# Optimization experiments

Hardware: AMD Instinct MI355X
Metric: run time of the kernel (lower is better)

The kernel has to match this reference:

```python
import jax, jax.numpy as jnp
import numpy as np

NUM_BANDS = 30
SPLIT_FREQ = 30
M_PARAM = 1
DIM = 2048
BATCH = 16384


def _dct_mat(N):
    # Orthonormal DCT-II matrix D: dct(x) = x @ D.T, idct(y) = y @ D
    n = np.arange(N, dtype=np.float64)
    kk = n[:, None]
    M = np.cos(np.pi * (n + 0.5) * kk / N)
    s = np.full(N, np.sqrt(2.0 / N))
    s[0] = np.sqrt(1.0 / N)
    return jnp.asarray((M * s[:, None]).astype(np.float32))


def _band_scale(freq_weights, k, N):
    # Precompute the per-frequency scale vector the torch loop applies band-by-band.
    pts = np.linspace(0, N - 1, NUM_BANDS + 1).astype(np.int64)  # torch .long() truncation
    scale = jnp.ones((N,), dtype=freq_weights.dtype)
    for i in range(NUM_BANDS):
        s, e = int(pts[i]), int(pts[i + 1])
        if e <= SPLIT_FREQ:
            f = 1.0 + freq_weights[i] * k * (1.0 - i / NUM_BANDS)
        else:
            f = 1.0 - freq_weights[i] * k * (1.0 - (i - NUM_BANDS // M_PARAM) / NUM_BANDS)
        scale = scale.at[s:e].set(f)  # bands are disjoint; base is 1
    return scale


def setup_inputs() -> dict:
    key = jax.random.key(0)
    ks = jax.random.split(key, 6)
    g = 0.02  # small init like xavier_uniform with gain 0.5
    return {
        "x": jax.random.normal(ks[0], (BATCH, DIM), dtype=jnp.float32),
        "freq_weights": jnp.ones((NUM_BANDS,), dtype=jnp.float32),
        "k": jnp.float32(0.3),
        "W1": jax.random.normal(ks[1], (1024, DIM), dtype=jnp.float32) * g,
        "b1": jnp.zeros((1024,), dtype=jnp.float32),
        "W2": jax.random.normal(ks[2], (512, 1024), dtype=jnp.float32) * g,
        "b2": jnp.zeros((512,), dtype=jnp.float32),
        "Wmu": jax.random.normal(ks[3], (256, 512), dtype=jnp.float32) * g,
        "bmu": jnp.zeros((256,), dtype=jnp.float32),
        "Wlv": jax.random.normal(ks[4], (256, 512), dtype=jnp.float32) * g,
        "blv": jnp.zeros((256,), dtype=jnp.float32),
    }


def reference(x, freq_weights, k, W1, b1, W2, b2, Wmu, bmu, Wlv, blv):
    N = x.shape[-1]
    D = _dct_mat(N)
    # DCT -> per-band reweight -> IDCT, fused as two matmuls and one vector multiply
    xd = (x @ D.T) * _band_scale(freq_weights, k, N)
    xe = xd @ D
    h = jax.nn.relu(xe @ W1.T + b1)
    h = jax.nn.relu(h @ W2.T + b2)
    mu = h @ Wmu.T + bmu
    logvar = h @ Wlv.T + blv
    return (mu, logvar)
```

## Files before the change

kernel.cpp:

```cpp
#include <hip/hip_runtime.h>
#include <hip/hip_bf16.h>
#include <math.h>

#define DIM 2048
#define BATCH 16384

typedef __attribute__((ext_vector_type(8))) short short8;
typedef __attribute__((ext_vector_type(4))) short short4v;
typedef __attribute__((ext_vector_type(4))) float floatx4;
typedef unsigned short ushort_t;

__device__ __forceinline__ ushort_t f2bf(float f) {
    union { float f; unsigned u; } v; v.f = f;
    unsigned r = v.u + 0x7FFFu + ((v.u >> 16) & 1u);
    return (ushort_t)(r >> 16);
}

__global__ void k_scale(const float* __restrict__ fw, const float* __restrict__ kp,
                        float* __restrict__ s) {
    int n = blockIdx.x * blockDim.x + threadIdx.x;
    if (n >= DIM) return;
    float kv = kp[0];
    float f = 1.0f;
    for (int i = 0; i < 30; ++i) {
        long s0 = (long)((double)i       * (double)(DIM - 1) / 30.0);
        long e0 = (long)((double)(i + 1) * (double)(DIM - 1) / 30.0);
        if (n >= s0 && n < e0) {
            if (e0 <= 30)
                f = 1.0f + fw[i] * kv * (1.0f - (float)i / 30.0f);
            else
                f = 1.0f - fw[i] * kv * (1.0f - (float)(i - 30) / 30.0f);
        }
    }
    s[n] = f;
}

__global__ void k_gen_d(ushort_t* __restrict__ D, ushort_t* __restrict__ Dt) {
    int idx = blockIdx.x * blockDim.x + threadIdx.x;
    int r = idx >> 11;
    int c = idx & (DIM - 1);
    const float w  = 7.6699039394282058e-4f;
    const float s0 = 0.02209708691207961f;
    const float s1 = 0.03125f;
    int m1 = ((2 * c + 1) * r) & (4 * DIM - 1);
    int m2 = ((2 * r + 1) * c) & (4 * DIM - 1);
    float v1 = __cosf(w * (float)m1) * (r == 0 ? s0 : s1);
    float v2 = __cosf(w * (float)m2) * (c == 0 ? s0 : s1);
    D[idx]  = f2bf(v1);
    Dt[idx] = f2bf(v2);
}

#define U_W1   262144
#define U_W2    65536
#define U_WH    16384
__global__ void k_cast_w(const float* __restrict__ W1, const float* __restrict__ W2,
                         const float* __restrict__ Wmu, const float* __restrict__ Wlv,
                         ushort_t* __restrict__ W1bf, ushort_t* __restrict__ W2bf,
                         ushort_t* __restrict__ Wcat) {
    int i = blockIdx.x * blockDim.x + threadIdx.x;
    const float* src; ushort_t* dst; int u;
    if (i < U_W1)                    { src = W1;  dst = W1bf;             u = i; }
    else if (i < U_W1 + U_W2)        { src = W2;  dst = W2bf;             u = i - U_W1; }
    else if (i < U_W1 + U_W2 + U_WH) { src = Wmu; dst = Wcat;             u = i - U_W1 - U_W2; }
    else                             { src = Wlv; dst = Wcat + 8 * U_WH;  u = i - U_W1 - U_W2 - U_WH; }
    const float4* p = reinterpret_cast<const float4*>(src) + 2 * (size_t)u;
    float4 a = p[0], b = p[1];
    short8 r;
    r[0] = (short)f2bf(a.x); r[1] = (short)f2bf(a.y);
    r[2] = (short)f2bf(a.z); r[3] = (short)f2bf(a.w);
    r[4] = (short)f2bf(b.x); r[5] = (short)f2bf(b.y);
    r[6] = (short)f2bf(b.z); r[7] = (short)f2bf(b.w);
    *reinterpret_cast<short8*>(dst + 8 * (size_t)u) = r;
}

__global__ void k_cast_x(const float* __restrict__ in, ushort_t* __restrict__ out) {
    int i = blockIdx.x * blockDim.x + threadIdx.x;
    const float4* p = reinterpret_cast<const float4*>(in) + 2 * (size_t)i;
    float4 a = p[0], b = p[1];
    short8 r;
    r[0] = (short)f2bf(a.x); r[1] = (short)f2bf(a.y);
    r[2] = (short)f2bf(a.z); r[3] = (short)f2bf(a.w);
    r[4] = (short)f2bf(b.x); r[5] = (short)f2bf(b.y);
    r[6] = (short)f2bf(b.z); r[7] = (short)f2bf(b.w);
    *reinterpret_cast<short8*>(out + 8 * (size_t)i) = r;
}

__global__ void k_red(const float* __restrict__ P, ushort_t* __restrict__ out,
                      const float* __restrict__ scale, int n4, int n4row) {
    int i = blockIdx.x * blockDim.x + threadIdx.x;
    const float4* p = reinterpret_cast<const float4*>(P);
    float4 a = p[i], b = p[i + n4], c = p[i + 2 * n4], d = p[i + 3 * n4];
    float4 s;
    s.x = a.x + b.x + c.x + d.x;
    s.y = a.y + b.y + c.y + d.y;
    s.z = a.z + b.z + c.z + d.z;
    s.w = a.w + b.w + c.w + d.w;
    if (scale) {
        float4 sc = reinterpret_cast<const float4*>(scale)[i & (n4row - 1)];
        s.x *= sc.x; s.y *= sc.y; s.z *= sc.z; s.w *= sc.w;
    }
    short4v o;
    o[0] = (short)f2bf(s.x); o[1] = (short)f2bf(s.y);
    o[2] = (short)f2bf(s.z); o[3] = (short)f2bf(s.w);
    *reinterpret_cast<short4v*>(out + 4 * (size_t)i) = o;
}

template<int TM, int TN, int BK, int EPI, bool SK4>
__device__ __forceinline__ void gemm_core(
        const ushort_t* __restrict__ A, const ushort_t* __restrict__ B,
        ushort_t* __restrict__ Cb, float* __restrict__ Cf,
        const float* __restrict__ ep0, const float* __restrict__ ep1,
        int M, int N, int K, int KC) {
    constexpr int BM = 32 * TM;
    constexpr int BN = 32 * TN;
    constexpr int SEGS = BK / 8;
    constexpr int RSH  = (BK == 32) ? 1 : 0;
    constexpr int SSH  = (SEGS == 4) ? 2 : 3;
    __shared__ __align__(16) ushort_t As[BM * BK];
    __shared__ __align__(16) ushort_t Bs[BN * BK];

    const int tid  = threadIdx.x;
    const int lane = tid & 63;
    const int wave = tid >> 6;
    const int wm   = wave >> 1;
    const int wn   = wave & 1;
    const int q    = lane >> 4;
    const int l16  = lane & 15;

    const int tilesM = M / BM;
    const int tilesN = N / BN;
    int bid = (int)blockIdx.x;
    int sk = 0;
    if constexpr (SK4) { int nt = tilesM * tilesN; sk = bid / nt; bid = bid % nt; }
    const int xcd = bid & 7;
    const int j   = bid >> 3;
    const int bm  = xcd * (tilesM >> 3) + j / tilesN;
    const int bn  = j % tilesN;

    floatx4 acc[TM][TN];
    #pragma unroll
    for (int i = 0; i < TM; ++i)
        #pragma unroll
        for (int jj = 0; jj < TN; ++jj)
            acc[i][jj] = (floatx4){0.f, 0.f, 0.f, 0.f};

    const long aBase = (long)bm * BM * K + (long)sk * KC;
    const long bBase = (long)bn * BN * K + (long)sk * KC;
    const int  KLOOP = SK4 ? KC : K;

    for (int kt = 0; kt < KLOOP; kt += BK) {
        __syncthreads();
        #pragma unroll
        for (int i = 0; i < BM * BK / 2048; ++i) {
            int idx = tid + i * 256;
            int row = idx >> SSH, seg = idx & (SEGS - 1);
            int gseg = seg ^ ((row >> RSH) & (SEGS - 1));
            const ushort_t* g = A + aBase + (long)row * K + kt + gseg * 8;
            __builtin_amdgcn_global_load_lds(
                (const __attribute__((address_space(1))) void*)g,
                (__attribute__((address_space(3))) void*)(As + idx * 8),
                16, 0, 0);
        }
        #pragma unroll
        for (int i = 0; i < BN * BK / 2048; ++i) {
            int idx = tid + i * 256;
            int row = idx >> SSH, seg = idx & (SEGS - 1);
            int gseg = seg ^ ((row >> RSH) & (SEGS - 1));
            const ushort_t* g = B + bBase + (long)row * K + kt + gseg * 8;
            __builtin_amdgcn_global_load_lds(
                (const __attribute__((address_space(1))) void*)g,
                (__attribute__((address_space(3))) void*)(Bs + idx * 8),
                16, 0, 0);
        }
        __syncthreads();

        #pragma unroll
        for (int ks = 0; ks < BK / 32; ++ks) {
            short8 af[TM], bfr[TN];
            #pragma unroll
            for (int t = 0; t < TM; ++t) {
                int srow = wm * TM * 16 + t * 16 + l16;
                int rseg = (ks * 4 + q) ^ ((srow >> RSH) & (SEGS - 1));
                af[t] = *reinterpret_cast<const short8*>(&As[srow * BK + rseg * 8]);
            }
            #pragma unroll
            for (int t = 0; t < TN; ++t) {
                int srow = wn * TN * 16 + t * 16 + l16;
                int rseg = (ks * 4 + q) ^ ((srow >> RSH) & (SEGS - 1));
                bfr[t] = *reinterpret_cast<const short8*>(&Bs[srow * BK + rseg * 8]);
            }
            #pragma unroll
            for (int i = 0; i < TM; ++i)
                #pragma unroll
                for (int jj = 0; jj < TN; ++jj)
                    acc[i][jj] = __builtin_amdgcn_mfma_f32_16x16x32_bf16(
                        af[i], bfr[jj], acc[i][jj], 0, 0, 0);
        }
    }

    #pragma unroll
    for (int i = 0; i < TM; ++i) {
        #pragma unroll
        for (int jj = 0; jj < TN; ++jj) {
            #pragma unroll
            for (int r = 0; r < 4; ++r) {
                int row = bm * BM + wm * TM * 16 + i * 16 + q * 4 + r;
                int col = bn * BN + wn * TN * 16 + jj * 16 + l16;
                float v = acc[i][jj][r];
                if constexpr (EPI == 2) {
                    v += ep0[col];
                    v = v > 0.f ? v : 0.f;
                    Cb[(long)row * N + col] = f2bf(v);
                } else if constexpr (EPI == 3) {
                    const int half = N >> 1;
                    if (col < half)
                        Cf[(long)row * half + col] = v + ep0[col];
                    else
                        Cf[(long)M * half + (long)row * half + (col - half)] = v + ep1[col - half];
                } else {
                    Cf[(long)sk * M * N + (long)row * N + col] = v;
                }
            }
        }
    }
}


__global__ __launch_bounds__(512, 2) void g2_256(const ushort_t* __restrict__ A,
        const ushort_t* __restrict__ B, ushort_t* __restrict__ Cb,
        const float* __restrict__ bias, int M, int N, int K) {
    constexpr int BM = 256, BN = 256, BK = 32;
    __shared__ __align__(16) ushort_t As[4][BM * BK];
    __shared__ __align__(16) ushort_t Bs[4][BN * BK];

    const int tid  = threadIdx.x;
    const int lane = tid & 63;
    const int wave = tid >> 6;
    const int wm   = wave >> 2;
    const int wn   = wave & 3;
    const int q    = lane >> 4;
    const int l16  = lane & 15;

    const int tilesM = M / BM;
    const int tilesN = N / BN;
    int bid = (int)blockIdx.x;
    const int xcd = bid & 7;
    const int jb  = bid >> 3;
    const int bm  = xcd * (tilesM >> 3) + jb / tilesN;
    const int bn  = jb % tilesN;
    const int NT  = K / BK;

    const long aBase = (long)bm * BM * K;
    const long bBase = (long)bn * BN * K;

    floatx4 acc[8][4];
    #pragma unroll
    for (int i = 0; i < 8; ++i)
        #pragma unroll
        for (int j = 0; j < 4; ++j)
            acc[i][j] = (floatx4){0.f, 0.f, 0.f, 0.f};

#define STAGE_A(t) do { int _sl = (t) & 3;                                          \
        _Pragma("unroll")                                                           \
        for (int _g = 0; _g < 2; ++_g) {                                            \
            int _idx = _g * 512 + tid;                                              \
            int _row = _idx >> 2, _seg = _idx & 3;                                  \
            int _gs = _seg ^ ((_row >> 1) & 3);                                     \
            const ushort_t* _gp = A + aBase + (long)_row * K + (t) * BK + _gs * 8;  \
            __builtin_amdgcn_global_load_lds(                                       \
                (const __attribute__((address_space(1))) void*)_gp,                 \
                (__attribute__((address_space(3))) void*)(&As[_sl][_idx * 8]),      \
                16, 0, 0);                                                          \
        } } while (0)
#define STAGE_B(t) do { int _sl = (t) & 3;                                          \
        _Pragma("unroll")                                                           \
        for (int _g = 0; _g < 2; ++_g) {                                            \
            int _idx = _g * 512 + tid;                                              \
            int _row = _idx >> 2, _seg = _idx & 3;                                  \
            int _gs = _seg ^ ((_row >> 1) & 3);                                     \
            const ushort_t* _gp = B + bBase + (long)_row * K + (t) * BK + _gs * 8;  \
            __builtin_amdgcn_global_load_lds(                                       \
                (const __attribute__((address_space(1))) void*)_gp,                 \
                (__attribute__((address_space(3))) void*)(&Bs[_sl][_idx * 8]),      \
                16, 0, 0);                                                          \
        } } while (0)

    STAGE_A(0); STAGE_B(0);
    STAGE_A(1); STAGE_B(1);
    STAGE_A(2); STAGE_B(2);
    asm volatile("s_waitcnt vmcnt(8)" ::: "memory");
    __builtin_amdgcn_s_barrier();
    asm volatile("" ::: "memory");

#define KTILE(tt, DOSTAGE, WAITOP) do {                                             \
        const int _slot = (tt) & 3;                                                 \
        short8 _bf[4], _alo[4], _ahi[4];                                            \
        _Pragma("unroll")                                                           \
        for (int _j = 0; _j < 4; ++_j) {                                            \
            int _sr = wn * 64 + _j * 16 + l16;                                      \
            int _rs = q ^ ((_sr >> 1) & 3);                                         \
            _bf[_j] = *reinterpret_cast<const short8*>(&Bs[_slot][_sr * BK + _rs * 8]); \
        }                                                                           \
        _Pragma("unroll")                                                           \
        for (int _i = 0; _i < 4; ++_i) {                                            \
            int _sr = wm * 128 + _i * 16 + l16;                                     \
            int _rs = q ^ ((_sr >> 1) & 3);                                         \
            _alo[_i] = *reinterpret_cast<const short8*>(&As[_slot][_sr * BK + _rs * 8]); \
        }                                                                           \
        _Pragma("unroll")                                                           \
        for (int _i = 0; _i < 4; ++_i) {                                            \
            int _sr = wm * 128 + 64 + _i * 16 + l16;                                \
            int _rs = q ^ ((_sr >> 1) & 3);                                         \
            _ahi[_i] = *reinterpret_cast<const short8*>(&As[_slot][_sr * BK + _rs * 8]); \
        }                                                                           \
        if (DOSTAGE) { STAGE_A((tt) + 3); STAGE_B((tt) + 3); }                      \
        __builtin_amdgcn_s_setprio(1);                                              \
        _Pragma("unroll")                                                           \
        for (int _i = 0; _i < 4; ++_i)                                              \
            _Pragma("unroll")                                                       \
            for (int _j = 0; _j < 4; ++_j)                                          \
                acc[_i][_j] = __builtin_amdgcn_mfma_f32_16x16x32_bf16(              \
                    _alo[_i], _bf[_j], acc[_i][_j], 0, 0, 0);                       \
        _Pragma("unroll")                                                           \
        for (int _i = 0; _i < 4; ++_i)                                              \
            _Pragma("unroll")                                                       \
            for (int _j = 0; _j < 4; ++_j)                                          \
                acc[4 + _i][_j] = __builtin_amdgcn_mfma_f32_16x16x32_bf16(          \
                    _ahi[_i], _bf[_j], acc[4 + _i][_j], 0, 0, 0);                   \
        __builtin_amdgcn_s_setprio(0);                                              \
        asm volatile("s_waitcnt lgkmcnt(0)" ::: "memory");                          \
        __builtin_amdgcn_sched_barrier(0);                                          \
        WAITOP;                                                                     \
        __builtin_amdgcn_s_barrier();                                               \
        asm volatile("" ::: "memory");                                              \
    } while (0)

    int t = 0;
    for (; t < NT - 3; ++t) {
        KTILE(t, true, asm volatile("s_waitcnt vmcnt(8)" ::: "memory"));
    }
    KTILE(t, false, asm volatile("s_waitcnt vmcnt(4)" ::: "memory")); ++t;
    KTILE(t, false, asm volatile("s_waitcnt vmcnt(0)" ::: "memory")); ++t;
    KTILE(t, false, (void)0);

#undef KTILE
#undef STAGE_A
#undef STAGE_B

    float bsv[4];
    #pragma unroll
    for (int j = 0; j < 4; ++j)
        bsv[j] = bias[bn * BN + wn * 64 + j * 16 + l16];
    #pragma unroll
    for (int i = 0; i < 8; ++i) {
        int row = bm * BM + wm * 128 + i * 16 + q * 4;
        #pragma unroll
        for (int j = 0; j < 4; ++j) {
            int col = bn * BN + wn * 64 + j * 16 + l16;
            #pragma unroll
            for (int r = 0; r < 4; ++r) {
                float v = acc[i][j][r] + bsv[j];
                v = v > 0.f ? v : 0.f;
                Cb[(long)(row + r) * N + col] = f2bf(v);
            }
        }
    }
}

template<int EPI>
__device__ __forceinline__ void gemm128_v2(
        const ushort_t* __restrict__ A, const ushort_t* __restrict__ B,
        ushort_t* __restrict__ Cb, float* __restrict__ Cf,
        const float* __restrict__ ep0, const float* __restrict__ ep1,
        int M, int N, int K) {
    constexpr int BM = 128, BN = 128, BK = 32;
    __shared__ __align__(16) ushort_t As[4][BM * BK];
    __shared__ __align__(16) ushort_t Bs[4][BN * BK];

    const int tid  = threadIdx.x;
    const int lane = tid & 63;
    const int wave = tid >> 6;
    const int wm   = wave >> 1;
    const int wn   = wave & 1;
    const int q    = lane >> 4;
    const int l16  = lane & 15;

    const int tilesM = M / BM;
    const int tilesN = N / BN;
    int bid = (int)blockIdx.x;
    const int xcd = bid & 7;
    const int jb  = bid >> 3;
    const int bm  = xcd * (tilesM >> 3) + jb / tilesN;
    const int bn  = jb % tilesN;
    const int NT  = K / BK;

    const long aBase = (long)bm * BM * K;
    const long bBase = (long)bn * BN * K;

    floatx4 acc[4][4];
    #pragma unroll
    for (int i = 0; i < 4; ++i)
        #pragma unroll
        for (int j = 0; j < 4; ++j)
            acc[i][j] = (floatx4){0.f, 0.f, 0.f, 0.f};

#define STAGE_A(t) do { int _sl = (t) & 3;                                          \
        _Pragma("unroll")                                                           \
        for (int _g = 0; _g < 2; ++_g) {                                            \
            int _idx = _g * 256 + tid;                                              \
            int _row = _idx >> 2, _seg = _idx & 3;                                  \
            int _gs = _seg ^ ((_row >> 1) & 3);                                     \
            const ushort_t* _gp = A + aBase + (long)_row * K + (t) * BK + _gs * 8;  \
            __builtin_amdgcn_global_load_lds(                                       \
                (const __attribute__((address_space(1))) void*)_gp,                 \
                (__attribute__((address_space(3))) void*)(&As[_sl][_idx * 8]),      \
                16, 0, 0);                                                          \
        } } while (0)
#define STAGE_B(t) do { int _sl = (t) & 3;                                          \
        _Pragma("unroll")                                                           \
        for (int _g = 0; _g < 2; ++_g) {                                            \
            int _idx = _g * 256 + tid;                                              \
            int _row = _idx >> 2, _seg = _idx & 3;                                  \
            int _gs = _seg ^ ((_row >> 1) & 3);                                     \
            const ushort_t* _gp = B + bBase + (long)_row * K + (t) * BK + _gs * 8;  \
            __builtin_amdgcn_global_load_lds(                                       \
                (const __attribute__((address_space(1))) void*)_gp,                 \
                (__attribute__((address_space(3))) void*)(&Bs[_sl][_idx * 8]),      \
                16, 0, 0);                                                          \
        } } while (0)

    STAGE_A(0); STAGE_B(0);
    STAGE_A(1); STAGE_B(1);
    STAGE_A(2); STAGE_B(2);
    asm volatile("s_waitcnt vmcnt(8)" ::: "memory");
    __builtin_amdgcn_s_barrier();
    asm volatile("" ::: "memory");

#define KTILE(tt, DOSTAGE, WAITOP) do {                                             \
        const int _slot = (tt) & 3;                                                 \
        short8 _bf[4], _af[4];                                                      \
        _Pragma("unroll")                                                           \
        for (int _j = 0; _j < 4; ++_j) {                                            \
            int _sr = wn * 64 + _j * 16 + l16;                                      \
            int _rs = q ^ ((_sr >> 1) & 3);                                         \
            _bf[_j] = *reinterpret_cast<const short8*>(&Bs[_slot][_sr * BK + _rs * 8]); \
        }                                                                           \
        _Pragma("unroll")                                                           \
        for (int _i = 0; _i < 4; ++_i) {                                            \
            int _sr = wm * 64 + _i * 16 + l16;                                      \
            int _rs = q ^ ((_sr >> 1) & 3);                                         \
            _af[_i] = *reinterpret_cast<const short8*>(&As[_slot][_sr * BK + _rs * 8]); \
        }                                                                           \
        if (DOSTAGE) { STAGE_A((tt) + 3); STAGE_B((tt) + 3); }                      \
        __builtin_amdgcn_s_setprio(1);                                              \
        _Pragma("unroll")                                                           \
        for (int _i = 0; _i < 4; ++_i)                                              \
            _Pragma("unroll")                                                       \
            for (int _j = 0; _j < 4; ++_j)                                          \
                acc[_i][_j] = __builtin_amdgcn_mfma_f32_16x16x32_bf16(              \
                    _af[_i], _bf[_j], acc[_i][_j], 0, 0, 0);                        \
        __builtin_amdgcn_s_setprio(0);                                              \
        asm volatile("s_waitcnt lgkmcnt(0)" ::: "memory");                          \
        __builtin_amdgcn_sched_barrier(0);                                          \
        WAITOP;                                                                     \
        __builtin_amdgcn_s_barrier();                                               \
        asm volatile("" ::: "memory");                                              \
    } while (0)

    int t = 0;
    for (; t < NT - 3; ++t) {
        KTILE(t, true, asm volatile("s_waitcnt vmcnt(8)" ::: "memory"));
    }
    KTILE(t, false, asm volatile("s_waitcnt vmcnt(4)" ::: "memory")); ++t;
    KTILE(t, false, asm volatile("s_waitcnt vmcnt(0)" ::: "memory")); ++t;
    KTILE(t, false, (void)0);

#undef KTILE
#undef STAGE_A
#undef STAGE_B

    #pragma unroll
    for (int i = 0; i < 4; ++i) {
        #pragma unroll
        for (int jj = 0; jj < 4; ++jj) {
            #pragma unroll
            for (int r = 0; r < 4; ++r) {
                int row = bm * BM + wm * 64 + i * 16 + q * 4 + r;
                int col = bn * BN + wn * 64 + jj * 16 + l16;
                float v = acc[i][jj][r];
                if constexpr (EPI == 2) {
                    v += ep0[col];
                    v = v > 0.f ? v : 0.f;
                    Cb[(long)row * N + col] = f2bf(v);
                } else {
                    const int half = N >> 1;
                    v += (col < half) ? ep0[col] : ep1[col - half];
                    if (col < half)
                        Cf[(long)row * half + col] = v;
                    else
                        Cf[(long)M * half + (long)row * half + (col - half)] = v;
                }
            }
        }
    }
}

__global__ __launch_bounds__(256) void g0p_sk(const ushort_t* A, const ushort_t* B,
        float* P, int M, int N, int K, int KC) {
    gemm_core<4, 4, 32, 4, true>(A, B, nullptr, P, nullptr, nullptr, M, N, K, KC);
}
__global__ __launch_bounds__(256) void g1p_sk(const ushort_t* A, const ushort_t* B,
        float* P, int M, int N, int K, int KC) {
    gemm_core<4, 4, 32, 4, true>(A, B, nullptr, P, nullptr, nullptr, M, N, K, KC);
}
__global__ __launch_bounds__(256, 2) void g3_h2(const ushort_t* A, const ushort_t* B,
        ushort_t* Cb, const float* ep0, int M, int N, int K) {
    gemm128_v2<2>(A, B, Cb, nullptr, ep0, nullptr, M, N, K);
}
__global__ __launch_bounds__(256, 2) void g4_head(const ushort_t* A, const ushort_t* B,
        float* Cf, const float* ep0, const float* ep1, int M, int N, int K) {
    gemm128_v2<3>(A, B, nullptr, Cf, ep0, ep1, M, N, K);
}

extern "C" void kernel_launch(void* const* d_in, const int* in_sizes, int n_in,
                              void* d_out, int out_size, void* d_ws, size_t ws_size,
                              hipStream_t stream) {
    const float* x   = (const float*)d_in[0];
    const float* fw  = (const float*)d_in[1];
    const float* kp  = (const float*)d_in[2];
    const float* W1  = (const float*)d_in[3];
    const float* b1  = (const float*)d_in[4];
    const float* W2  = (const float*)d_in[5];
    const float* b2  = (const float*)d_in[6];
    const float* Wmu = (const float*)d_in[7];
    const float* bmu = (const float*)d_in[8];
    const float* Wlv = (const float*)d_in[9];
    const float* blv = (const float*)d_in[10];
    float* out = (float*)d_out;

    char* ws = (char*)d_ws;
    const size_t MB = 1024 * 1024;
    ushort_t* W1bf = (ushort_t*)(ws + 0);
    ushort_t* Dbf  = (ushort_t*)(ws + 4   * MB);
    ushort_t* Dtbf = (ushort_t*)(ws + 12  * MB);
    ushort_t* T1sT = (ushort_t*)(ws + 20  * MB);
    ushort_t* H1   = (ushort_t*)(ws + 0);
    float*    P    = (float*)   (ws + 32  * MB);
    ushort_t* Xbf  = (ushort_t*)(ws + 32  * MB);
    ushort_t* H2   = (ushort_t*)(ws + 96  * MB);
    ushort_t* M1T  = (ushort_t*)(ws + 112 * MB);
    ushort_t* W2bf = (ushort_t*)(ws + 116 * MB);
    ushort_t* Wcat = (ushort_t*)(ws + 117 * MB);
    float*    svec = (float*)   (ws + 118 * MB);

    hipLaunchKernelGGL(k_scale, dim3(DIM / 256), dim3(256), 0, stream, fw, kp, svec);
    hipLaunchKernelGGL(k_gen_d, dim3(DIM * DIM / 256), dim3(256), 0, stream, Dbf, Dtbf);
    hipLaunchKernelGGL(k_cast_w, dim3((U_W1 + U_W2 + 2 * U_WH) / 256), dim3(256), 0, stream,
                       W1, W2, Wmu, Wlv, W1bf, W2bf, Wcat);

    hipLaunchKernelGGL(g0p_sk, dim3(8 * 16 * 4), dim3(256), 0, stream,
                       W1bf, Dbf, P, 1024, 2048, 2048, 512);
    hipLaunchKernelGGL(k_red, dim3(1024 * 2048 / 4 / 256), dim3(256), 0, stream,
                       P, T1sT, svec, 1024 * 2048 / 4, 2048 / 4);
    hipLaunchKernelGGL(g1p_sk, dim3(8 * 16 * 4), dim3(256), 0, stream,
                       T1sT, Dtbf, P, 1024, 2048, 2048, 512);
    hipLaunchKernelGGL(k_red, dim3(1024 * 2048 / 4 / 256), dim3(256), 0, stream,
                       P, M1T, nullptr, 1024 * 2048 / 4, 2048 / 4);

    hipLaunchKernelGGL(k_cast_x, dim3(BATCH * DIM / 8 / 256), dim3(256), 0, stream, x, Xbf);

    hipLaunchKernelGGL(g2_256, dim3((BATCH / 256) * (1024 / 256)), dim3(512), 0, stream,
                       Xbf, M1T, H1, b1, BATCH, 1024, 2048);
    hipLaunchKernelGGL(g3_h2, dim3((BATCH / 128) * (512 / 128)), dim3(256), 0, stream,
                       H1, W2bf, H2, b2, BATCH, 512, 1024);
    hipLaunchKernelGGL(g4_head, dim3((BATCH / 128) * (512 / 128)), dim3(256), 0, stream,
                       H2, Wcat, out, bmu, blv, BATCH, 512, 512);

    (void)in_sizes; (void)n_in; (void)out_size; (void)ws_size;
}
```

Before: 377.3 us.

## Double-buffer LDS fragment reads to overlap with MFMAs in 256x256 GEMM

Splits the k-tile body into read, MFMA and sync macros and holds two register sets of A/B fragments. The LDS reads for tile t+1 are issued before the MFMAs of tile t, and the vmcnt wait is loosened so the next-next stage can land while computing. This aims to hide LDS read latency behind matrix-core work. It doubles the fragment register footprint and hardcodes the tail for exactly 64 k-tiles (K = 2048).

After: 392.9 us. 1.04x slower.

```diff
diff --git a/kernel.cpp b/kernel.cpp
--- a/kernel.cpp
+++ b/kernel.cpp
@@ -225,7 +225,6 @@
     }
 }
 
-
 __global__ __launch_bounds__(512, 2) void g2_256(const ushort_t* __restrict__ A,
         const ushort_t* __restrict__ B, ushort_t* __restrict__ Cb,
         const float* __restrict__ bias, int M, int N, int K) {
@@ -285,65 +284,97 @@
                 16, 0, 0);                                                          \
         } } while (0)
 
+#define READF(tt, BF, ALO, AHI) do { const int _slot = (tt) & 3;                    \
+        _Pragma("unroll")                                                           \
+        for (int _j = 0; _j < 4; ++_j) {                                            \
+            int _sr = wn * 64 + _j * 16 + l16;                                      \
+            int _rs = q ^ ((_sr >> 1) & 3);                                         \
+            BF[_j] = *reinterpret_cast<const short8*>(&Bs[_slot][_sr * BK + _rs * 8]); \
+        }                                                                           \
+        _Pragma("unroll")                                                           \
+        for (int _i = 0; _i < 4; ++_i) {                                            \
+            int _sr = wm * 128 + _i * 16 + l16;                                     \
+            int _rs = q ^ ((_sr >> 1) & 3);                                         \
+            ALO[_i] = *reinterpret_cast<const short8*>(&As[_slot][_sr * BK + _rs * 8]); \
+        }                                                                           \
+        _Pragma("unroll")                                                           \
+        for (int _i = 0; _i < 4; ++_i) {                                            \
+            int _sr = wm * 128 + 64 + _i * 16 + l16;                                \
+            int _rs = q ^ ((_sr >> 1) & 3);                                         \
+            AHI[_i] = *reinterpret_cast<const short8*>(&As[_slot][_sr * BK + _rs * 8]); \
+        }                                                                           \
+    } while (0)
+
+#define MFMA_SET(BF, ALO, AHI) do {                                                 \
+        __builtin_amdgcn_s_setprio(1);                                              \
+        _Pragma("unroll")                                                           \
+        for (int _i = 0; _i < 4; ++_i)                                              \
+            _Pragma("unroll")                                                       \
+            for (int _j = 0; _j < 4; ++_j)                                          \
+                acc[_i][_j] = __builtin_amdgcn_mfma_f32_16x16x32_bf16(              \
+                    ALO[_i], BF[_j], acc[_i][_j], 0, 0, 0);                         \
+        _Pragma("unroll")                                                           \
+        for (int _i = 0; _i < 4; ++_i)                                              \
+            _Pragma("unroll")                                                       \
+            for (int _j = 0; _j < 4; ++_j)                                          \
+                acc[4 + _i][_j] = __builtin_amdgcn_mfma_f32_16x16x32_bf16(          \
+                    AHI[_i], BF[_j], acc[4 + _i][_j], 0, 0, 0);                     \
+        __builtin_amdgcn_s_setprio(0);                                              \
+    } while (0)
+
+#define ENDSYNC4  do { asm volatile("s_waitcnt lgkmcnt(0)" ::: "memory");           \
+        __builtin_amdgcn_sched_barrier(0);                                          \
+        asm volatile("s_waitcnt vmcnt(4)" ::: "memory");                            \
+        __builtin_amdgcn_s_barrier(); asm volatile("" ::: "memory"); } while (0)
+#define ENDSYNC0  do { asm volatile("s_waitcnt lgkmcnt(0)" ::: "memory");           \
+        __builtin_amdgcn_sched_barrier(0);                                          \
+        asm volatile("s_waitcnt vmcnt(0)" ::: "memory");                            \
+        __builtin_amdgcn_s_barrier(); asm volatile("" ::: "memory"); } while (0)
+#define ENDSYNCL  do { asm volatile("s_waitcnt lgkmcnt(0)" ::: "memory");           \
+        __builtin_amdgcn_sched_barrier(0);                                          \
+        __builtin_amdgcn_s_barrier(); asm volatile("" ::: "memory"); } while (0)
+
+    short8 bf0[4], alo0[4], ahi0[4];
+    short8 bf1[4], alo1[4], ahi1[4];
+
     STAGE_A(0); STAGE_B(0);
     STAGE_A(1); STAGE_B(1);
     STAGE_A(2); STAGE_B(2);
     asm volatile("s_waitcnt vmcnt(8)" ::: "memory");
     __builtin_amdgcn_s_barrier();
     asm volatile("" ::: "memory");
-
-#define KTILE(tt, DOSTAGE, WAITOP) do {                                             \
-        const int _slot = (tt) & 3;                                                 \
-        short8 _bf[4], _alo[4], _ahi[4];                                            \
-        _Pragma("unroll")                                                           \
-        for (int _j = 0; _j < 4; ++_j) {                                            \
-            int _sr = wn * 64 + _j * 16 + l16;                                      \
-            int _rs = q ^ ((_sr >> 1) & 3);                                         \
-            _bf[_j] = *reinterpret_cast<const short8*>(&Bs[_slot][_sr * BK + _rs * 8]); \
-        }                                                                           \
-        _Pragma("unroll")                                                           \
-        for (int _i = 0; _i < 4; ++_i) {                                            \
-            int _sr = wm * 128 + _i * 16 + l16;                                     \
-            int _rs = q ^ ((_sr >> 1) & 3);                                         \
-            _alo[_i] = *reinterpret_cast<const short8*>(&As[_slot][_sr * BK + _rs * 8]); \
-        }                                                                           \
-        _Pragma("unroll")                                                           \
-        for (int _i = 0; _i < 4; ++_i) {                                            \
-            int _sr = wm * 128 + 64 + _i * 16 + l16;                                \
-            int _rs = q ^ ((_sr >> 1) & 3);                                         \
-            _ahi[_i] = *reinterpret_cast<const short8*>(&As[_slot][_sr * BK + _rs * 8]); \
-        }                                                                           \
-        if (DOSTAGE) { STAGE_A((tt) + 3); STAGE_B((tt) + 3); }                      \
-        __builtin_amdgcn_s_setprio(1);                                              \
-        _Pragma("unroll")                                                           \
-        for (int _i = 0; _i < 4; ++_i)                                              \
-            _Pragma("unroll")                                                       \
-            for (int _j = 0; _j < 4; ++_j)                                          \
-                acc[_i][_j] = __builtin_amdgcn_mfma_f32_16x16x32_bf16(              \
-                    _alo[_i], _bf[_j], acc[_i][_j], 0, 0, 0);                       \
-        _Pragma("unroll")                                                           \
-        for (int _i = 0; _i < 4; ++_i)                                              \
-            _Pragma("unroll")                                                       \
-            for (int _j = 0; _j < 4; ++_j)                                          \
-                acc[4 + _i][_j] = __builtin_amdgcn_mfma_f32_16x16x32_bf16(          \
-                    _ahi[_i], _bf[_j], acc[4 + _i][_j], 0, 0, 0);                   \
-        __builtin_amdgcn_s_setprio(0);                                              \
-        asm volatile("s_waitcnt lgkmcnt(0)" ::: "memory");                          \
-        __builtin_amdgcn_sched_barrier(0);                                          \
-        WAITOP;                                                                     \
-        __builtin_amdgcn_s_barrier();                                               \
-        asm volatile("" ::: "memory");                                              \
-    } while (0)
-
-    int t = 0;
-    for (; t < NT - 3; ++t) {
-        KTILE(t, true, asm volatile("s_waitcnt vmcnt(8)" ::: "memory"));
-    }
-    KTILE(t, false, asm volatile("s_waitcnt vmcnt(4)" ::: "memory")); ++t;
-    KTILE(t, false, asm volatile("s_waitcnt vmcnt(0)" ::: "memory")); ++t;
-    KTILE(t, false, (void)0);
-
-#undef KTILE
+    READF(0, bf0, alo0, ahi0);
+    asm volatile("s_waitcnt vmcnt(4)" ::: "memory");
+    __builtin_amdgcn_s_barrier();
+    asm volatile("" ::: "memory");
+
+    for (int t = 0; t < NT - 4; t += 2) {
+        READF(t + 1, bf1, alo1, ahi1);
+        STAGE_A(t + 3); STAGE_B(t + 3);
+        MFMA_SET(bf0, alo0, ahi0);
+        ENDSYNC4;
+        READF(t + 2, bf0, alo0, ahi0);
+        STAGE_A(t + 4); STAGE_B(t + 4);
+        MFMA_SET(bf1, alo1, ahi1);
+        ENDSYNC4;
+    }
+    READF(61, bf1, alo1, ahi1);
+    STAGE_A(63); STAGE_B(63);
+    MFMA_SET(bf0, alo0, ahi0);
+    ENDSYNC4;
+    READF(62, bf0, alo0, ahi0);
+    MFMA_SET(bf1, alo1, ahi1);
+    ENDSYNC0;
+    READF(63, bf1, alo1, ahi1);
+    MFMA_SET(bf0, alo0, ahi0);
+    ENDSYNCL;
+    MFMA_SET(bf1, alo1, ahi1);
+
+#undef ENDSYNCL
+#undef ENDSYNC0
+#undef ENDSYNC4
+#undef MFMA_SET
+#undef READF
 #undef STAGE_A
 #undef STAGE_B
 
```

## Restructure g2_256 to BK=64 double buffer with four-phase ping-pong MFMA schedule

Applied to the files above, without the earlier changes.

Raises the K tile of the 256x256 bf16 GEMM from 32 to 64, switches from a 4-slot to a 2-slot LDS ring, and changes the swizzle to XOR over 8 segments. Each K tile is split into four sub-phases, each doing an LDS fragment read and an MFMA quadrant, separated by barriers. Global-to-LDS staging for tile t+2 is interleaved between the phases. The aim is fewer barrier round trips per unit of K and better overlap of loads with MFMA, at the cost of more barriers per tile and a shallower prefetch distance.

Result: slower. 386.0 us (+2.3%).

```diff
diff --git a/kernel.cpp b/kernel.cpp
--- a/kernel.cpp
+++ b/kernel.cpp
@@ -225,13 +225,12 @@
     }
 }
 
-
 __global__ __launch_bounds__(512, 2) void g2_256(const ushort_t* __restrict__ A,
         const ushort_t* __restrict__ B, ushort_t* __restrict__ Cb,
         const float* __restrict__ bias, int M, int N, int K) {
-    constexpr int BM = 256, BN = 256, BK = 32;
-    __shared__ __align__(16) ushort_t As[4][BM * BK];
-    __shared__ __align__(16) ushort_t Bs[4][BN * BK];
+    constexpr int BM = 256, BN = 256, BK = 64;
+    __shared__ __align__(16) ushort_t As[2][BM * BK];
+    __shared__ __align__(16) ushort_t Bs[2][BN * BK];
 
     const int tid  = threadIdx.x;
     const int lane = tid & 63;
@@ -260,92 +259,119 @@
         for (int j = 0; j < 4; ++j)
             acc[i][j] = (floatx4){0.f, 0.f, 0.f, 0.f};
 
-#define STAGE_A(t) do { int _sl = (t) & 3;                                          \
+#define STG_A(h, tt) do {                                                           \
         _Pragma("unroll")                                                           \
         for (int _g = 0; _g < 2; ++_g) {                                            \
             int _idx = _g * 512 + tid;                                              \
-            int _row = _idx >> 2, _seg = _idx & 3;                                  \
-            int _gs = _seg ^ ((_row >> 1) & 3);                                     \
-            const ushort_t* _gp = A + aBase + (long)_row * K + (t) * BK + _gs * 8;  \
+            int _r = _idx >> 3, _s = _idx & 7;                                      \
+            int _gs = _s ^ (_r & 7);                                                \
+            const ushort_t* _gp = A + aBase + (long)((h) * 128 + _r) * K            \
+                                  + (tt) * BK + _gs * 8;                            \
             __builtin_amdgcn_global_load_lds(                                       \
                 (const __attribute__((address_space(1))) void*)_gp,                 \
-                (__attribute__((address_space(3))) void*)(&As[_sl][_idx * 8]),      \
+                (__attribute__((address_space(3))) void*)                           \
+                    (&As[(tt) & 1][(h) * 8192 + _idx * 8]),                         \
                 16, 0, 0);                                                          \
         } } while (0)
-#define STAGE_B(t) do { int _sl = (t) & 3;                                          \
+#define STG_B(h, tt) do {                                                           \
         _Pragma("unroll")                                                           \
         for (int _g = 0; _g < 2; ++_g) {                                            \
             int _idx = _g * 512 + tid;                                              \
-            int _row = _idx >> 2, _seg = _idx & 3;                                  \
-            int _gs = _seg ^ ((_row >> 1) & 3);                                     \
-            const ushort_t* _gp = B + bBase + (long)_row * K + (t) * BK + _gs * 8;  \
+            int _r = _idx >> 3, _s = _idx & 7;                                      \
+            int _gs = _s ^ (_r & 7);                                                \
+            const ushort_t* _gp = B + bBase + (long)((h) * 128 + _r) * K            \
+                                  + (tt) * BK + _gs * 8;                            \
             __builtin_amdgcn_global_load_lds(                                       \
                 (const __attribute__((address_space(1))) void*)_gp,                 \
-                (__attribute__((address_space(3))) void*)(&Bs[_sl][_idx * 8]),      \
+                (__attribute__((address_space(3))) void*)                           \
+                    (&Bs[(tt) & 1][(h) * 8192 + _idx * 8]),                         \
                 16, 0, 0);                                                          \
         } } while (0)
 
-    STAGE_A(0); STAGE_B(0);
-    STAGE_A(1); STAGE_B(1);
-    STAGE_A(2); STAGE_B(2);
+#define RDA(dst, IB) do {                                                           \
+        _Pragma("unroll")                                                           \
+        for (int _i = 0; _i < 4; ++_i)                                              \
+            _Pragma("unroll")                                                       \
+            for (int _k = 0; _k < 2; ++_k) {                                        \
+                int _sr = wm * 128 + ((IB) + _i) * 16 + l16;                        \
+                int _rs = (_k * 4 + q) ^ (_sr & 7);                                 \
+                dst[_i][_k] = *reinterpret_cast<const short8*>(                     \
+                    &As[_buf][_sr * BK + _rs * 8]);                                 \
+            } } while (0)
+#define RDB(dst, JB) do {                                                           \
+        _Pragma("unroll")                                                           \
+        for (int _j = 0; _j < 2; ++_j)                                              \
+            _Pragma("unroll")                                                       \
+            for (int _k = 0; _k < 2; ++_k) {                                        \
+                int _sr = wn * 64 + ((JB) + _j) * 16 + l16;                         \
+                int _rs = (_k * 4 + q) ^ (_sr & 7);                                 \
+                dst[_j][_k] = *reinterpret_cast<const short8*>(                     \
+                    &Bs[_buf][_sr * BK + _rs * 8]);                                 \
+            } } while (0)
+
+#define MM(AF, BF, IB, JB) do {                                                     \
+        __builtin_amdgcn_s_setprio(1);                                              \
+        _Pragma("unroll")                                                           \
+        for (int _k = 0; _k < 2; ++_k)                                              \
+            _Pragma("unroll")                                                       \
+            for (int _i = 0; _i < 4; ++_i)                                          \
+                _Pragma("unroll")                                                   \
+                for (int _j = 0; _j < 2; ++_j)                                      \
+                    acc[(IB) + _i][(JB) + _j] =                                     \
+                        __builtin_amdgcn_mfma_f32_16x16x32_bf16(                    \
+                            AF[_i][_k], BF[_j][_k],                                 \
+                            acc[(IB) + _i][(JB) + _j], 0, 0, 0);                    \
+        __builtin_amdgcn_s_setprio(0);                                              \
+    } while (0)
+
+#define MID do { __builtin_amdgcn_s_barrier();                                      \
+        asm volatile("s_waitcnt lgkmcnt(0)" ::: "memory");                          \
+        __builtin_amdgcn_sched_barrier(0); } while (0)
+#define ENDP do { __builtin_amdgcn_s_barrier();                                     \
+        asm volatile("" ::: "memory"); } while (0)
+
+    STG_A(0, 0); STG_A(1, 0); STG_B(0, 0); STG_B(1, 0);
+    STG_A(0, 1); STG_A(1, 1); STG_B(0, 1); STG_B(1, 1);
     asm volatile("s_waitcnt vmcnt(8)" ::: "memory");
     __builtin_amdgcn_s_barrier();
     asm volatile("" ::: "memory");
 
-#define KTILE(tt, DOSTAGE, WAITOP) do {                                             \
-        const int _slot = (tt) & 3;                                                 \
-        short8 _bf[4], _alo[4], _ahi[4];                                            \
-        _Pragma("unroll")                                                           \
-        for (int _j = 0; _j < 4; ++_j) {                                            \
-            int _sr = wn * 64 + _j * 16 + l16;                                      \
-            int _rs = q ^ ((_sr >> 1) & 3);                                         \
-            _bf[_j] = *reinterpret_cast<const short8*>(&Bs[_slot][_sr * BK + _rs * 8]); \
-        }                                                                           \
-        _Pragma("unroll")                                                           \
-        for (int _i = 0; _i < 4; ++_i) {                                            \
-            int _sr = wm * 128 + _i * 16 + l16;                                     \
-            int _rs = q ^ ((_sr >> 1) & 3);                                         \
-            _alo[_i] = *reinterpret_cast<const short8*>(&As[_slot][_sr * BK + _rs * 8]); \
-        }                                                                           \
-        _Pragma("unroll")                                                           \
-        for (int _i = 0; _i < 4; ++_i) {                                            \
-            int _sr = wm * 128 + 64 + _i * 16 + l16;                                \
-            int _rs = q ^ ((_sr >> 1) & 3);                                         \
-            _ahi[_i] = *reinterpret_cast<const short8*>(&As[_slot][_sr * BK + _rs * 8]); \
-        }                                                                           \
-        if (DOSTAGE) { STAGE_A((tt) + 3); STAGE_B((tt) + 3); }                      \
-        __builtin_amdgcn_s_setprio(1);                                              \
-        _Pragma("unroll")                                                           \
-        for (int _i = 0; _i < 4; ++_i)                                              \
-            _Pragma("unroll")                                                       \
-            for (int _j = 0; _j < 4; ++_j)                                          \
-                acc[_i][_j] = __builtin_amdgcn_mfma_f32_16x16x32_bf16(              \
-                    _alo[_i], _bf[_j], acc[_i][_j], 0, 0, 0);                       \
-        _Pragma("unroll")                                                           \
-        for (int _i = 0; _i < 4; ++_i)                                              \
-            _Pragma("unroll")                                                       \
-            for (int _j = 0; _j < 4; ++_j)                                          \
-                acc[4 + _i][_j] = __builtin_amdgcn_mfma_f32_16x16x32_bf16(          \
-                    _ahi[_i], _bf[_j], acc[4 + _i][_j], 0, 0, 0);                   \
-        __builtin_amdgcn_s_setprio(0);                                              \
-        asm volatile("s_waitcnt lgkmcnt(0)" ::: "memory");                          \
-        __builtin_amdgcn_sched_barrier(0);                                          \
-        WAITOP;                                                                     \
-        __builtin_amdgcn_s_barrier();                                               \
-        asm volatile("" ::: "memory");                                              \
-    } while (0)
-
-    int t = 0;
-    for (; t < NT - 3; ++t) {
-        KTILE(t, true, asm volatile("s_waitcnt vmcnt(8)" ::: "memory"));
-    }
-    KTILE(t, false, asm volatile("s_waitcnt vmcnt(4)" ::: "memory")); ++t;
-    KTILE(t, false, asm volatile("s_waitcnt vmcnt(0)" ::: "memory")); ++t;
-    KTILE(t, false, (void)0);
-
-#undef KTILE
-#undef STAGE_A
-#undef STAGE_B
+    short8 alo[4][2], ahi[4][2], blo[2][2], bhi[2][2];
+
+    for (int t = 0; t < NT; ++t) {
+        const int _buf = t & 1;
+        RDA(alo, 0);
+        RDB(blo, 0);
+        MID;
+        MM(alo, blo, 0, 0);
+        ENDP;
+        RDB(bhi, 2);
+        MID;
+        MM(alo, bhi, 0, 2);
+        ENDP;
+        RDA(ahi, 4);
+        if (t < NT - 2) { STG_B(0, t + 2); STG_B(1, t + 2); }
+        MID;
+        MM(ahi, blo, 4, 0);
+        ENDP;
+        if (t < NT - 2) { STG_A(0, t + 2); STG_A(1, t + 2); }
+        __builtin_amdgcn_s_barrier();
+        asm volatile("" ::: "memory");
+        MM(ahi, bhi, 4, 2);
+        if (t < NT - 2)
+            asm volatile("s_waitcnt vmcnt(8)" ::: "memory");
+        else if (t == NT - 2)
+            asm volatile("s_waitcnt vmcnt(0)" ::: "memory");
+        ENDP;
+    }
+
+#undef ENDP
+#undef MID
+#undef MM
+#undef RDB
+#undef RDA
+#undef STG_B
+#undef STG_A
 
     float bsv[4];
     #pragma unroll
```

## Fuse fp32-to-bf16 cast of x into the first GEMM's A-tile loading

Applied to the files above, without the earlier changes.

Removes the separate k_cast_x pass and the bf16 copy of x. The first MLP GEMM now loads fp32 x into registers, converts to bf16 and writes it to LDS itself, while B keeps the async global-to-LDS path. The A-tile pipeline becomes register-staged, with conversion placed two tiles ahead and loads three tiles ahead. This saves a 128 MB read plus 64 MB write round trip. In exchange the GEMM reads twice as many A bytes, holds more registers and does the conversion work itself.

Result: no change. 376.7 us (-0.2%).

```diff
diff --git a/kernel.cpp b/kernel.cpp
--- a/kernel.cpp
+++ b/kernel.cpp
@@ -73,18 +73,6 @@
     *reinterpret_cast<short8*>(dst + 8 * (size_t)u) = r;
 }
 
-__global__ void k_cast_x(const float* __restrict__ in, ushort_t* __restrict__ out) {
-    int i = blockIdx.x * blockDim.x + threadIdx.x;
-    const float4* p = reinterpret_cast<const float4*>(in) + 2 * (size_t)i;
-    float4 a = p[0], b = p[1];
-    short8 r;
-    r[0] = (short)f2bf(a.x); r[1] = (short)f2bf(a.y);
-    r[2] = (short)f2bf(a.z); r[3] = (short)f2bf(a.w);
-    r[4] = (short)f2bf(b.x); r[5] = (short)f2bf(b.y);
-    r[6] = (short)f2bf(b.z); r[7] = (short)f2bf(b.w);
-    *reinterpret_cast<short8*>(out + 8 * (size_t)i) = r;
-}
-
 __global__ void k_red(const float* __restrict__ P, ushort_t* __restrict__ out,
                       const float* __restrict__ scale, int n4, int n4row) {
     int i = blockIdx.x * blockDim.x + threadIdx.x;
@@ -225,8 +213,7 @@
     }
 }
 
-
-__global__ __launch_bounds__(512, 2) void g2_256(const ushort_t* __restrict__ A,
+__global__ __launch_bounds__(512, 2) void g2f(const float* __restrict__ Xf,
         const ushort_t* __restrict__ B, ushort_t* __restrict__ Cb,
         const float* __restrict__ bias, int M, int N, int K) {
     constexpr int BM = 256, BN = 256, BK = 32;
@@ -260,92 +247,101 @@
         for (int j = 0; j < 4; ++j)
             acc[i][j] = (floatx4){0.f, 0.f, 0.f, 0.f};
 
-#define STAGE_A(t) do { int _sl = (t) & 3;                                          \
+    float4 rA[4];
+
+#define LDA(tt) do {                                                                \
         _Pragma("unroll")                                                           \
         for (int _g = 0; _g < 2; ++_g) {                                            \
             int _idx = _g * 512 + tid;                                              \
             int _row = _idx >> 2, _seg = _idx & 3;                                  \
             int _gs = _seg ^ ((_row >> 1) & 3);                                     \
-            const ushort_t* _gp = A + aBase + (long)_row * K + (t) * BK + _gs * 8;  \
-            __builtin_amdgcn_global_load_lds(                                       \
-                (const __attribute__((address_space(1))) void*)_gp,                 \
-                (__attribute__((address_space(3))) void*)(&As[_sl][_idx * 8]),      \
-                16, 0, 0);                                                          \
+            const float4* _p = reinterpret_cast<const float4*>(                     \
+                Xf + aBase + (long)_row * K + (tt) * BK + _gs * 8);                 \
+            rA[2 * _g]     = _p[0];                                                 \
+            rA[2 * _g + 1] = _p[1];                                                 \
         } } while (0)
-#define STAGE_B(t) do { int _sl = (t) & 3;                                          \
+
+#define CVW(tt) do { const int _sl = (tt) & 3;                                      \
+        _Pragma("unroll")                                                           \
+        for (int _g = 0; _g < 2; ++_g) {                                            \
+            int _idx = _g * 512 + tid;                                              \
+            float4 _a = rA[2 * _g], _b = rA[2 * _g + 1];                            \
+            short8 _o;                                                              \
+            _o[0] = (short)f2bf(_a.x); _o[1] = (short)f2bf(_a.y);                   \
+            _o[2] = (short)f2bf(_a.z); _o[3] = (short)f2bf(_a.w);                   \
+            _o[4] = (short)f2bf(_b.x); _o[5] = (short)f2bf(_b.y);                   \
+            _o[6] = (short)f2bf(_b.z); _o[7] = (short)f2bf(_b.w);                   \
+            *reinterpret_cast<short8*>(&As[_sl][_idx * 8]) = _o;                    \
+        } } while (0)
+
+#define STG_B(tt) do { const int _sl = (tt) & 3;                                    \
         _Pragma("unroll")                                                           \
         for (int _g = 0; _g < 2; ++_g) {                                            \
             int _idx = _g * 512 + tid;                                              \
             int _row = _idx >> 2, _seg = _idx & 3;                                  \
             int _gs = _seg ^ ((_row >> 1) & 3);                                     \
-            const ushort_t* _gp = B + bBase + (long)_row * K + (t) * BK + _gs * 8;  \
+            const ushort_t* _gp = B + bBase + (long)_row * K + (tt) * BK + _gs * 8; \
             __builtin_amdgcn_global_load_lds(                                       \
                 (const __attribute__((address_space(1))) void*)_gp,                 \
                 (__attribute__((address_space(3))) void*)(&Bs[_sl][_idx * 8]),      \
                 16, 0, 0);                                                          \
         } } while (0)
 
-    STAGE_A(0); STAGE_B(0);
-    STAGE_A(1); STAGE_B(1);
-    STAGE_A(2); STAGE_B(2);
-    asm volatile("s_waitcnt vmcnt(8)" ::: "memory");
+    LDA(0); CVW(0);
+    LDA(1); CVW(1);
+    STG_B(0); STG_B(1); STG_B(2);
+    LDA(2);
+    asm volatile("s_waitcnt lgkmcnt(0)" ::: "memory");
+    asm volatile("s_waitcnt vmcnt(4)" ::: "memory");
     __builtin_amdgcn_s_barrier();
     asm volatile("" ::: "memory");
 
-#define KTILE(tt, DOSTAGE, WAITOP) do {                                             \
-        const int _slot = (tt) & 3;                                                 \
-        short8 _bf[4], _alo[4], _ahi[4];                                            \
-        _Pragma("unroll")                                                           \
-        for (int _j = 0; _j < 4; ++_j) {                                            \
-            int _sr = wn * 64 + _j * 16 + l16;                                      \
-            int _rs = q ^ ((_sr >> 1) & 3);                                         \
-            _bf[_j] = *reinterpret_cast<const short8*>(&Bs[_slot][_sr * BK + _rs * 8]); \
-        }                                                                           \
-        _Pragma("unroll")                                                           \
-        for (int _i = 0; _i < 4; ++_i) {                                            \
-            int _sr = wm * 128 + _i * 16 + l16;                                     \
-            int _rs = q ^ ((_sr >> 1) & 3);                                         \
-            _alo[_i] = *reinterpret_cast<const short8*>(&As[_slot][_sr * BK + _rs * 8]); \
-        }                                                                           \
-        _Pragma("unroll")                                                           \
-        for (int _i = 0; _i < 4; ++_i) {                                            \
-            int _sr = wm * 128 + 64 + _i * 16 + l16;                                \
-            int _rs = q ^ ((_sr >> 1) & 3);                                         \
-            _ahi[_i] = *reinterpret_cast<const short8*>(&As[_slot][_sr * BK + _rs * 8]); \
-        }                                                                           \
-        if (DOSTAGE) { STAGE_A((tt) + 3); STAGE_B((tt) + 3); }                      \
-        __builtin_amdgcn_s_setprio(1);                                              \
-        _Pragma("unroll")                                                           \
-        for (int _i = 0; _i < 4; ++_i)                                              \
-            _Pragma("unroll")                                                       \
-            for (int _j = 0; _j < 4; ++_j)                                          \
-                acc[_i][_j] = __builtin_amdgcn_mfma_f32_16x16x32_bf16(              \
-                    _alo[_i], _bf[_j], acc[_i][_j], 0, 0, 0);                       \
-        _Pragma("unroll")                                                           \
-        for (int _i = 0; _i < 4; ++_i)                                              \
-            _Pragma("unroll")                                                       \
-            for (int _j = 0; _j < 4; ++_j)                                          \
-                acc[4 + _i][_j] = __builtin_amdgcn_mfma_f32_16x16x32_bf16(          \
-                    _ahi[_i], _bf[_j], acc[4 + _i][_j], 0, 0, 0);                   \
-        __builtin_amdgcn_s_setprio(0);                                              \
-        asm volatile("s_waitcnt lgkmcnt(0)" ::: "memory");                          \
-        __builtin_amdgcn_sched_barrier(0);                                          \
-        WAITOP;                                                                     \
-        __builtin_amdgcn_s_barrier();                                               \
-        asm volatile("" ::: "memory");                                              \
-    } while (0)
-
-    int t = 0;
-    for (; t < NT - 3; ++t) {
-        KTILE(t, true, asm volatile("s_waitcnt vmcnt(8)" ::: "memory"));
-    }
-    KTILE(t, false, asm volatile("s_waitcnt vmcnt(4)" ::: "memory")); ++t;
-    KTILE(t, false, asm volatile("s_waitcnt vmcnt(0)" ::: "memory")); ++t;
-    KTILE(t, false, (void)0);
-
-#undef KTILE
-#undef STAGE_A
-#undef STAGE_B
+    for (int t = 0; t < NT; ++t) {
+        const int slot = t & 3;
+        if (t + 2 < NT) CVW(t + 2);
+        short8 bf[4], alo[4], ahi[4];
+        #pragma unroll
+        for (int j = 0; j < 4; ++j) {
+            int sr = wn * 64 + j * 16 + l16;
+            int rs = q ^ ((sr >> 1) & 3);
+            bf[j] = *reinterpret_cast<const short8*>(&Bs[slot][sr * BK + rs * 8]);
+        }
+        #pragma unroll
+        for (int i = 0; i < 4; ++i) {
+            int sr = wm * 128 + i * 16 + l16;
+            int rs = q ^ ((sr >> 1) & 3);
+            alo[i] = *reinterpret_cast<const short8*>(&As[slot][sr * BK + rs * 8]);
+        }
+        #pragma unroll
+        for (int i = 0; i < 4; ++i) {
+            int sr = wm * 128 + 64 + i * 16 + l16;
+            int rs = q ^ ((sr >> 1) & 3);
+            ahi[i] = *reinterpret_cast<const short8*>(&As[slot][sr * BK + rs * 8]);
+        }
+        if (t + 3 < NT) { STG_B(t + 3); LDA(t + 3); }
+        __builtin_amdgcn_s_setprio(1);
+        #pragma unroll
+        for (int i = 0; i < 4; ++i)
+            #pragma unroll
+            for (int j = 0; j < 4; ++j)
+                acc[i][j] = __builtin_amdgcn_mfma_f32_16x16x32_bf16(
+                    alo[i], bf[j], acc[i][j], 0, 0, 0);
+        #pragma unroll
+        for (int i = 0; i < 4; ++i)
+            #pragma unroll
+            for (int j = 0; j < 4; ++j)
+                acc[4 + i][j] = __builtin_amdgcn_mfma_f32_16x16x32_bf16(
+                    ahi[i], bf[j], acc[4 + i][j], 0, 0, 0);
+        __builtin_amdgcn_s_setprio(0);
+        asm volatile("s_waitcnt lgkmcnt(0)" ::: "memory");
+        __builtin_amdgcn_sched_barrier(0);
+        __builtin_amdgcn_s_barrier();
+        asm volatile("" ::: "memory");
+    }
+
+#undef STG_B
+#undef CVW
+#undef LDA
 
     float bsv[4];
     #pragma unroll
@@ -546,7 +542,6 @@
     ushort_t* T1sT = (ushort_t*)(ws + 20  * MB);
     ushort_t* H1   = (ushort_t*)(ws + 0);
     float*    P    = (float*)   (ws + 32  * MB);
-    ushort_t* Xbf  = (ushort_t*)(ws + 32  * MB);
     ushort_t* H2   = (ushort_t*)(ws + 96  * MB);
     ushort_t* M1T  = (ushort_t*)(ws + 112 * MB);
     ushort_t* W2bf = (ushort_t*)(ws + 116 * MB);
@@ -567,10 +562,8 @@
     hipLaunchKernelGGL(k_red, dim3(1024 * 2048 / 4 / 256), dim3(256), 0, stream,
                        P, M1T, nullptr, 1024 * 2048 / 4, 2048 / 4);
 
-    hipLaunchKernelGGL(k_cast_x, dim3(BATCH * DIM / 8 / 256), dim3(256), 0, stream, x, Xbf);
-
-    hipLaunchKernelGGL(g2_256, dim3((BATCH / 256) * (1024 / 256)), dim3(512), 0, stream,
-                       Xbf, M1T, H1, b1, BATCH, 1024, 2048);
+    hipLaunchKernelGGL(g2f, dim3((BATCH / 256) * (1024 / 256)), dim3(512), 0, stream,
+                       x, M1T, H1, b1, BATCH, 1024, 2048);
     hipLaunchKernelGGL(g3_h2, dim3((BATCH / 128) * (512 / 128)), dim3(256), 0, stream,
                        H1, W2bf, H2, b2, BATCH, 512, 1024);
     hipLaunchKernelGGL(g4_head, dim3((BATCH / 128) * (512 / 128)), dim3(256), 0, stream,
```
